# Optimization experiments

Measured on AMD Instinct MI355X. Metric: run time of the kernel, lower is better.

The kernel has to match this reference:

```python
import jax, jax.numpy as jnp
import numpy as np

THR = 1.0     # snntorch Leaky default threshold
BETA = 0.9    # args.beta
ALPHA = 2.0   # surrogate.atan default alpha

@jax.custom_vjp
def atan_spike(x):
    # Heaviside forward, arctan surrogate gradient (snntorch surrogate.atan)
    return (x > 0).astype(x.dtype)

def _aspk_fwd(x):
    return atan_spike(x), x

def _aspk_bwd(x, g):
    return (g * (ALPHA / 2.0) / (1.0 + (jnp.pi / 2.0 * ALPHA * x) ** 2),)

atan_spike.defvjp(_aspk_fwd, _aspk_bwd)

def setup_inputs() -> dict:
    key = jax.random.key(0)
    k = jax.random.split(key, 5)
    B, D, H, C = 32768, 187, 50, 5
    return {
        "x": jax.random.normal(k[0], (B, D), dtype=jnp.float32),
        "W1": jax.random.normal(k[1], (H, D), dtype=jnp.float32) * (1.0 / np.sqrt(D)),
        "b1": jax.random.normal(k[2], (H,), dtype=jnp.float32) * 0.01,
        "W2": jax.random.normal(k[3], (C, H), dtype=jnp.float32) * (1.0 / np.sqrt(H)),
        "b2": jax.random.normal(k[4], (C,), dtype=jnp.float32) * 0.01,
        "num_steps": 100,
    }

def reference(x, W1, b1, W2, b2, num_steps):
    B = x.shape[0]
    dt = x.dtype
    # fc1(x) is identical every timestep (x is static), compute once
    cur1 = x @ W1.T + b1  # [B, 50]

    def step(carry, _):
        mem1, mem2 = carry
        # Leaky: reset computed from PREVIOUS mem (detached), subtract mechanism
        reset1 = jax.lax.stop_gradient((mem1 > THR).astype(dt))
        mem1 = BETA * mem1 + cur1 - reset1 * THR
        spk1 = atan_spike(mem1 - THR)
        cur2 = spk1 @ W2.T + b2  # [B, num_classes]
        reset2 = jax.lax.stop_gradient((mem2 > THR).astype(dt))
        mem2 = BETA * mem2 + cur2 - reset2 * THR
        spk2 = atan_spike(mem2 - THR)
        return (mem1, mem2), (spk2, mem2)

    init = (jnp.zeros((B, W1.shape[0]), dt), jnp.zeros((B, W2.shape[0]), dt))
    _, (spk_rec, mem_rec) = jax.lax.scan(step, init, None, length=num_steps)
    return spk_rec, mem_rec  # each [num_steps, B, num_classes]
```

## Files before the change

kernel.cpp:

```cpp
#include <hip/hip_runtime.h>

typedef float v2f __attribute__((ext_vector_type(2)));
typedef float f4  __attribute__((ext_vector_type(4)));

#define DD   187
#define HH   50
#define PH   56
#define HPJ  14
#define NP   7
#define NC   5
#define RPB  64
#define BLK  256
#define DCH  64
#define NCHUNK 3
#define BETA 0.9f
#define GRP  16
#define SLAB (RPB * NC)
#define LDSF (2 * GRP * SLAB)

__device__ __forceinline__ float dpp_xor1(float v) {
    return __builtin_bit_cast(float,
        __builtin_amdgcn_mov_dpp(__builtin_bit_cast(int, v), 0xB1, 0xF, 0xF, true));
}
__device__ __forceinline__ float dpp_xor2(float v) {
    return __builtin_bit_cast(float,
        __builtin_amdgcn_mov_dpp(__builtin_bit_cast(int, v), 0x4E, 0xF, 0xF, true));
}

__device__ __forceinline__ float spike1(float m) {
    float t = fmaf(m, 0x1.0p60f, -0x1.0p60f);
    return fminf(fmaxf(t, 0.f), 1.f);
}
__device__ __forceinline__ v2f spike2(v2f m) {
    const v2f BIG2  = { 0x1.0p60f,  0x1.0p60f};
    const v2f NBIG2 = {-0x1.0p60f, -0x1.0p60f};
    const v2f ONE2  = {1.f, 1.f};
    const v2f ZERO2 = {0.f, 0.f};
    v2f t = __builtin_elementwise_fma(m, BIG2, NBIG2);
    return __builtin_elementwise_min(__builtin_elementwise_max(t, ZERO2), ONE2);
}

__global__ __launch_bounds__(BLK, 2)
void snn_kernel(const float* __restrict__ x,
                const float* __restrict__ W1,
                const float* __restrict__ b1,
                const float* __restrict__ W2,
                const float* __restrict__ b2,
                const int*   __restrict__ nsp,
                float* __restrict__ out, int Brows)
{
    __shared__ alignas(16) float smem[LDSF];
    float* xs  = smem;
    float* w1t = smem + RPB * 65;
    float* spk_lds = smem;
    float* mem_lds = smem + GRP * SLAB;

    const int tid = threadIdx.x;
    const int p   = tid >> 2;
    const int k   = tid & 3;
    const int row0 = blockIdx.x * RPB;
    const int NS  = nsp[0];

    v2f acc[NP];
#pragma unroll
    for (int i = 0; i < NP; ++i) acc[i] = (v2f){0.f, 0.f};

    for (int ch = 0; ch < NCHUNK; ++ch) {
        const int d0 = ch * DCH;
        for (int i = tid; i < RPB * DCH; i += BLK) {
            int r = i >> 6, dd = i & 63;
            int d = d0 + dd;
            xs[r * 65 + dd] = (d < DD) ? x[(size_t)(row0 + r) * DD + d] : 0.f;
        }
        for (int i = tid; i < DCH * PH; i += BLK) {
            int h = i >> 6, dd = i & 63;
            int d = d0 + dd;
            w1t[dd * PH + h] = (h < HH && d < DD) ? W1[h * DD + d] : 0.f;
        }
        __syncthreads();

        const float* xr = xs + p * 65;
#pragma unroll 4
        for (int d = 0; d < DCH; ++d) {
            float xv = xr[d];
            const v2f* wr = (const v2f*)(w1t + d * PH + k * HPJ);
            v2f xvv = {xv, xv};
#pragma unroll
            for (int i = 0; i < NP; ++i)
                acc[i] = __builtin_elementwise_fma(xvv, wr[i], acc[i]);
        }
        __syncthreads();
    }

    v2f c1[NP];
#pragma unroll
    for (int i = 0; i < NP; ++i) {
        int h0 = k * HPJ + 2 * i;
        v2f bb = { (h0     < HH) ? b1[h0]     : 0.f,
                   (h0 + 1 < HH) ? b1[h0 + 1] : 0.f };
        c1[i] = acc[i] + bb;
    }

    v2f w2r[NC][NP];
#pragma unroll
    for (int c = 0; c < NC; ++c)
#pragma unroll
        for (int i = 0; i < NP; ++i) {
            int h0 = k * HPJ + 2 * i;
            w2r[c][i] = { (h0     < HH) ? W2[c * HH + h0]     : 0.f,
                          (h0 + 1 < HH) ? W2[c * HH + h0 + 1] : 0.f };
        }
    const float b2A = b2[k];
    const float b2B = b2[4];

    v2f m1[NP], s1[NP];
#pragma unroll
    for (int i = 0; i < NP; ++i) { m1[i] = (v2f){0.f, 0.f}; s1[i] = (v2f){0.f, 0.f}; }
    float mA = 0.f, sA = 0.f, mB = 0.f, sB = 0.f;

    const size_t stride = (size_t)Brows * NC;
    const int p5k = p * NC + k;
    const v2f BETA2 = {BETA, BETA};

    __syncthreads();

    int t0 = 0;
    while (t0 < NS) {
        const int steps = (NS - t0 < GRP) ? (NS - t0) : GRP;

        for (int u = 0; u < steps; ++u) {
            v2f cp[NC];
#pragma unroll
            for (int c = 0; c < NC; ++c) cp[c] = (v2f){0.f, 0.f};
#pragma unroll
            for (int i = 0; i < NP; ++i) {
                v2f m = __builtin_elementwise_fma(BETA2, m1[i], c1[i]) - s1[i];
                m1[i] = m;
                v2f s = spike2(m);
                s1[i] = s;
#pragma unroll
                for (int c = 0; c < NC; ++c)
                    cp[c] = __builtin_elementwise_fma(s, w2r[c][i], cp[c]);
            }
            float cur2[NC];
#pragma unroll
            for (int c = 0; c < NC; ++c) {
                float r = cp[c].x + cp[c].y;
                r += dpp_xor1(r);
                r += dpp_xor2(r);
                cur2[c] = r;
            }
            float cA = (k == 0) ? cur2[0] : (k == 1) ? cur2[1] : (k == 2) ? cur2[2] : cur2[3];
            float cB = cur2[4];

            mA = fmaf(BETA, mA, cA + b2A) - sA;
            sA = spike1(mA);
            mB = fmaf(BETA, mB, cB + b2B) - sB;
            sB = spike1(mB);

            spk_lds[u * SLAB + p5k] = sA;
            mem_lds[u * SLAB + p5k] = mA;
            if (k == 0) {
                spk_lds[u * SLAB + p * NC + 4] = sB;
                mem_lds[u * SLAB + p * NC + 4] = mB;
            }
        }

        __syncthreads();

        const int totalChunks = steps * (SLAB / 4);
        for (int c = tid; c < totalChunks; c += BLK) {
            int u   = c / (SLAB / 4);
            int pos = c - u * (SLAB / 4);
            f4 sv = *(const f4*)(spk_lds + u * SLAB + pos * 4);
            f4 mv = *(const f4*)(mem_lds + u * SLAB + pos * 4);
            float* sp = out + (size_t)(t0 + u) * stride + (size_t)row0 * NC + pos * 4;
            float* mp = sp + (size_t)NS * stride;
            *(f4*)sp = sv;
            *(f4*)mp = mv;
        }

        __syncthreads();
        t0 += steps;
    }
}

extern "C" void kernel_launch(void* const* d_in, const int* in_sizes, int n_in,
                              void* d_out, int out_size, void* d_ws, size_t ws_size,
                              hipStream_t stream) {
    const float* x  = (const float*)d_in[0];
    const float* W1 = (const float*)d_in[1];
    const float* b1 = (const float*)d_in[2];
    const float* W2 = (const float*)d_in[3];
    const float* b2 = (const float*)d_in[4];
    const int*   ns = (const int*)d_in[5];
    int B = in_sizes[0] / DD;
    int nblocks = B / RPB;
    snn_kernel<<<nblocks, BLK, 0, stream>>>(x, W1, b1, W2, b2, ns, (float*)d_out, B);
}
```

Measured before the change: 220.8 us.

## Split each row's hidden units across eight lanes and halve rows per block

Each batch row is now handled by 8 lanes, each owning 8 hidden units as two 4-wide vectors, instead of 4 lanes with 14 units. Rows per block drop from 64 to 32 and the launch-bounds occupancy hint rises from 2 to 4 blocks. This shortens the per-lane serial recurrence and doubles the block count, so more parallelism and latency hiding are available. In exchange the reduction needs a third DPP stage, and 3 of every 8 lanes do redundant output-neuron work whose results are discarded.

```diff
diff --git a/kernel.cpp b/kernel.cpp
--- a/kernel.cpp
+++ b/kernel.cpp
@@ -1,22 +1,23 @@
 #include <hip/hip_runtime.h>
 
 typedef float v2f __attribute__((ext_vector_type(2)));
-typedef float f4  __attribute__((ext_vector_type(4)));
+typedef float v4f __attribute__((ext_vector_type(4)));
 
 #define DD   187
 #define HH   50
-#define PH   56
-#define HPJ  14
-#define NP   7
+#define PH   64
+#define NPL  2
 #define NC   5
-#define RPB  64
+#define RPB  32
 #define BLK  256
 #define DCH  64
 #define NCHUNK 3
 #define BETA 0.9f
 #define GRP  16
 #define SLAB (RPB * NC)
-#define LDSF (2 * GRP * SLAB)
+#define PH1F (RPB * 65 + DCH * PH)
+#define SLABF (2 * GRP * SLAB)
+#define LDSF (PH1F > SLABF ? PH1F : SLABF)
 
 __device__ __forceinline__ float dpp_xor1(float v) {
     return __builtin_bit_cast(float,
@@ -26,21 +27,25 @@
     return __builtin_bit_cast(float,
         __builtin_amdgcn_mov_dpp(__builtin_bit_cast(int, v), 0x4E, 0xF, 0xF, true));
 }
+__device__ __forceinline__ float dpp_hmirror(float v) {
+    return __builtin_bit_cast(float,
+        __builtin_amdgcn_mov_dpp(__builtin_bit_cast(int, v), 0x141, 0xF, 0xF, true));
+}
 
 __device__ __forceinline__ float spike1(float m) {
     float t = fmaf(m, 0x1.0p60f, -0x1.0p60f);
     return fminf(fmaxf(t, 0.f), 1.f);
 }
-__device__ __forceinline__ v2f spike2(v2f m) {
-    const v2f BIG2  = { 0x1.0p60f,  0x1.0p60f};
-    const v2f NBIG2 = {-0x1.0p60f, -0x1.0p60f};
-    const v2f ONE2  = {1.f, 1.f};
-    const v2f ZERO2 = {0.f, 0.f};
-    v2f t = __builtin_elementwise_fma(m, BIG2, NBIG2);
-    return __builtin_elementwise_min(__builtin_elementwise_max(t, ZERO2), ONE2);
-}
-
-__global__ __launch_bounds__(BLK, 2)
+__device__ __forceinline__ v4f spike4(v4f m) {
+    const v4f BIG  = { 0x1.0p60f,  0x1.0p60f,  0x1.0p60f,  0x1.0p60f};
+    const v4f NBIG = {-0x1.0p60f, -0x1.0p60f, -0x1.0p60f, -0x1.0p60f};
+    const v4f ONE  = {1.f, 1.f, 1.f, 1.f};
+    const v4f ZERO = {0.f, 0.f, 0.f, 0.f};
+    v4f t = __builtin_elementwise_fma(m, BIG, NBIG);
+    return __builtin_elementwise_min(__builtin_elementwise_max(t, ZERO), ONE);
+}
+
+__global__ __launch_bounds__(BLK, 4)
 void snn_kernel(const float* __restrict__ x,
                 const float* __restrict__ W1,
                 const float* __restrict__ b1,
@@ -56,14 +61,14 @@
     float* mem_lds = smem + GRP * SLAB;
 
     const int tid = threadIdx.x;
-    const int p   = tid >> 2;
-    const int k   = tid & 3;
+    const int p   = tid >> 3;
+    const int o   = tid & 7;
     const int row0 = blockIdx.x * RPB;
     const int NS  = nsp[0];
 
-    v2f acc[NP];
-#pragma unroll
-    for (int i = 0; i < NP; ++i) acc[i] = (v2f){0.f, 0.f};
+    v4f acc[NPL];
+#pragma unroll
+    for (int i = 0; i < NPL; ++i) acc[i] = (v4f){0.f, 0.f, 0.f, 0.f};
 
     for (int ch = 0; ch < NCHUNK; ++ch) {
         const int d0 = ch * DCH;
@@ -83,44 +88,48 @@
 #pragma unroll 4
         for (int d = 0; d < DCH; ++d) {
             float xv = xr[d];
-            const v2f* wr = (const v2f*)(w1t + d * PH + k * HPJ);
-            v2f xvv = {xv, xv};
-#pragma unroll
-            for (int i = 0; i < NP; ++i)
+            const v4f* wr = (const v4f*)(w1t + d * PH + o * 8);
+            v4f xvv = {xv, xv, xv, xv};
+#pragma unroll
+            for (int i = 0; i < NPL; ++i)
                 acc[i] = __builtin_elementwise_fma(xvv, wr[i], acc[i]);
         }
         __syncthreads();
     }
 
-    v2f c1[NP];
-#pragma unroll
-    for (int i = 0; i < NP; ++i) {
-        int h0 = k * HPJ + 2 * i;
-        v2f bb = { (h0     < HH) ? b1[h0]     : 0.f,
-                   (h0 + 1 < HH) ? b1[h0 + 1] : 0.f };
+    v4f c1[NPL];
+#pragma unroll
+    for (int i = 0; i < NPL; ++i) {
+        v4f bb;
+#pragma unroll
+        for (int e = 0; e < 4; ++e) {
+            int h = o * 8 + 4 * i + e;
+            bb[e] = (h < HH) ? b1[h] : 0.f;
+        }
         c1[i] = acc[i] + bb;
     }
 
-    v2f w2r[NC][NP];
+    v4f w2r[NC][NPL];
 #pragma unroll
     for (int c = 0; c < NC; ++c)
 #pragma unroll
-        for (int i = 0; i < NP; ++i) {
-            int h0 = k * HPJ + 2 * i;
-            w2r[c][i] = { (h0     < HH) ? W2[c * HH + h0]     : 0.f,
-                          (h0 + 1 < HH) ? W2[c * HH + h0 + 1] : 0.f };
-        }
-    const float b2A = b2[k];
-    const float b2B = b2[4];
-
-    v2f m1[NP], s1[NP];
-#pragma unroll
-    for (int i = 0; i < NP; ++i) { m1[i] = (v2f){0.f, 0.f}; s1[i] = (v2f){0.f, 0.f}; }
-    float mA = 0.f, sA = 0.f, mB = 0.f, sB = 0.f;
+        for (int i = 0; i < NPL; ++i) {
+#pragma unroll
+            for (int e = 0; e < 4; ++e) {
+                int h = o * 8 + 4 * i + e;
+                w2r[c][i][e] = (h < HH) ? W2[c * HH + h] : 0.f;
+            }
+        }
+    const float b2own = b2[(o < NC) ? o : (NC - 1)];
+
+    v4f m1[NPL], s1[NPL];
+#pragma unroll
+    for (int i = 0; i < NPL; ++i) { m1[i] = (v4f){0,0,0,0}; s1[i] = (v4f){0,0,0,0}; }
+    float mo = 0.f, so = 0.f;
 
     const size_t stride = (size_t)Brows * NC;
-    const int p5k = p * NC + k;
-    const v2f BETA2 = {BETA, BETA};
+    const int lslot = p * NC + o;
+    const v4f BETA4 = {BETA, BETA, BETA, BETA};
 
     __syncthreads();
 
@@ -129,14 +138,14 @@
         const int steps = (NS - t0 < GRP) ? (NS - t0) : GRP;
 
         for (int u = 0; u < steps; ++u) {
-            v2f cp[NC];
-#pragma unroll
-            for (int c = 0; c < NC; ++c) cp[c] = (v2f){0.f, 0.f};
-#pragma unroll
-            for (int i = 0; i < NP; ++i) {
-                v2f m = __builtin_elementwise_fma(BETA2, m1[i], c1[i]) - s1[i];
+            v4f cp[NC];
+#pragma unroll
+            for (int c = 0; c < NC; ++c) cp[c] = (v4f){0,0,0,0};
+#pragma unroll
+            for (int i = 0; i < NPL; ++i) {
+                v4f m = __builtin_elementwise_fma(BETA4, m1[i], c1[i]) - s1[i];
                 m1[i] = m;
-                v2f s = spike2(m);
+                v4f s = spike4(m);
                 s1[i] = s;
 #pragma unroll
                 for (int c = 0; c < NC; ++c)
@@ -145,24 +154,27 @@
             float cur2[NC];
 #pragma unroll
             for (int c = 0; c < NC; ++c) {
-                float r = cp[c].x + cp[c].y;
+                v2f lo = {cp[c][0], cp[c][1]};
+                v2f hi = {cp[c][2], cp[c][3]};
+                v2f hs = lo + hi;
+                float r = hs.x + hs.y;
                 r += dpp_xor1(r);
                 r += dpp_xor2(r);
+                r += dpp_hmirror(r);
                 cur2[c] = r;
             }
-            float cA = (k == 0) ? cur2[0] : (k == 1) ? cur2[1] : (k == 2) ? cur2[2] : cur2[3];
-            float cB = cur2[4];
-
-            mA = fmaf(BETA, mA, cA + b2A) - sA;
-            sA = spike1(mA);
-            mB = fmaf(BETA, mB, cB + b2B) - sB;
-            sB = spike1(mB);
-
-            spk_lds[u * SLAB + p5k] = sA;
-            mem_lds[u * SLAB + p5k] = mA;
-            if (k == 0) {
-                spk_lds[u * SLAB + p * NC + 4] = sB;
-                mem_lds[u * SLAB + p * NC + 4] = mB;
+            float cown = cur2[0];
+            cown = (o == 1) ? cur2[1] : cown;
+            cown = (o == 2) ? cur2[2] : cown;
+            cown = (o == 3) ? cur2[3] : cown;
+            cown = (o == 4) ? cur2[4] : cown;
+
+            mo = fmaf(BETA, mo, cown + b2own) - so;
+            so = spike1(mo);
+
+            if (o < NC) {
+                spk_lds[u * SLAB + lslot] = so;
+                mem_lds[u * SLAB + lslot] = mo;
             }
         }
 
@@ -172,12 +184,12 @@
         for (int c = tid; c < totalChunks; c += BLK) {
             int u   = c / (SLAB / 4);
             int pos = c - u * (SLAB / 4);
-            f4 sv = *(const f4*)(spk_lds + u * SLAB + pos * 4);
-            f4 mv = *(const f4*)(mem_lds + u * SLAB + pos * 4);
+            v4f sv = *(const v4f*)(spk_lds + u * SLAB + pos * 4);
+            v4f mv = *(const v4f*)(mem_lds + u * SLAB + pos * 4);
             float* sp = out + (size_t)(t0 + u) * stride + (size_t)row0 * NC + pos * 4;
             float* mp = sp + (size_t)NS * stride;
-            *(f4*)sp = sv;
-            *(f4*)mp = mv;
+            *(v4f*)sp = sv;
+            *(v4f*)mp = mv;
         }
 
         __syncthreads();
```

Result: slower. 237.8 us (+7.7%).
